# Kernel tuning notes

Hardware: AMD Instinct MI355X
Metric: run time of the kernel (lower is better)

Reference implementation:

```python
import jax, jax.numpy as jnp
import numpy as np

B = 2048          # number of graphs in the batch
ACT_DIM = 14      # nodes per graph (act_dim)
C = 128           # in_channels
H = 256           # hidden_size


def _pair_edges(n):
    ii, jj = np.meshgrid(np.arange(n), np.arange(n), indexing='ij')
    m = ii != jj
    return np.stack([ii[m], jj[m]], axis=1)  # [n*(n-1), 2]


def setup_inputs() -> dict:
    key = jax.random.key(0)
    ks = jax.random.split(key, 12)
    edges_np = _pair_edges(ACT_DIM)                       # [182, 2]
    offs = (np.arange(B) * ACT_DIM)[:, None, None]
    batched = (edges_np[None] + offs).reshape(-1, 2)      # [B*182, 2]
    edge_index = jnp.asarray(batched.T, dtype=jnp.int64 if jax.config.jax_enable_x64 else jnp.int32)
    edges = jnp.asarray(edges_np, dtype=jnp.int32)

    def lin(k, o, i):
        return jax.random.normal(k, (o, i), jnp.float32) * (1.0 / np.sqrt(i))

    return {
        'state': jax.random.normal(ks[0], (B * ACT_DIM, C), jnp.float32),
        'conv_w': lin(ks[1], C, C),
        'conv_b': jnp.zeros((C,), jnp.float32),
        'lin1_w': lin(ks[2], H, 2 * C),
        'lin1_b': jax.random.normal(ks[3], (H,), jnp.float32) * 0.01,
        'lin2_w': lin(ks[4], H, H),
        'lin2_b': jax.random.normal(ks[5], (H,), jnp.float32) * 0.01,
        'mu_w': lin(ks[6], 1, H),
        'mu_b': jnp.zeros((1,), jnp.float32),
        'sig_w': lin(ks[7], 1, H),
        'sig_b': jnp.zeros((1,), jnp.float32),
        'noise': jax.random.normal(ks[8], (B, edges_np.shape[0]), jnp.float32),
        'edge_index': edge_index,
        'edges': edges,
    }


def _gcn_conv(x, edge_index, w, b):
    # Standard GCNConv: add self-loops, symmetric normalization, x @ W^T, scatter-add, + bias.
    n = x.shape[0]
    loops = jnp.arange(n, dtype=edge_index.dtype)
    src = jnp.concatenate([edge_index[0], loops])
    dst = jnp.concatenate([edge_index[1], loops])
    deg = jax.ops.segment_sum(jnp.ones_like(src, dtype=x.dtype), dst, num_segments=n)
    dinv = jax.lax.rsqrt(deg)  # deg >= 1 because of self-loops
    norm = dinv[src] * dinv[dst]                       # [E+N]
    xw = x @ w.T                                       # [N, C]
    msg = xw[src] * norm[:, None]                      # gather + scale
    return jax.ops.segment_sum(msg, dst, num_segments=n) + b


def reference(state, conv_w, conv_b, lin1_w, lin1_b, lin2_w, lin2_b,
              mu_w, mu_b, sig_w, sig_b, noise, edge_index, edges):
    out = jax.nn.relu(_gcn_conv(state, edge_index, conv_w, conv_b))
    x = (out + state).reshape(-1, ACT_DIM, C)          # [B, 14, C]
    es, ed = edges[:, 0], edges[:, 1]
    ef = jnp.concatenate([x[:, es, :], x[:, ed, :]], axis=2)   # [B, E, 2C]
    h = jax.nn.leaky_relu(jnp.einsum('bec,hc->beh', ef, lin1_w) + lin1_b)
    h = jax.nn.leaky_relu(jnp.einsum('beh,gh->beg', h, lin2_w) + lin2_b)
    mu = jax.nn.softplus(jnp.einsum('beh,oh->beo', h, mu_w) + mu_b)[..., 0]   # [B, E]
    std = jax.nn.softplus(jnp.einsum('beh,oh->beo', h, sig_w) + sig_b)[..., 0]
    action = mu + std * noise                          # Normal rsample with fixed eps
    log_prob = jnp.sum(
        -0.5 * ((action - mu) / std) ** 2 - jnp.log(std) - 0.5 * jnp.log(2.0 * jnp.pi),
        axis=-1)                                       # [B]
    return action, log_prob
```

## Files before the change

### kernel.cpp

```cpp
#include <hip/hip_runtime.h>

#define ACT 14
#define CC 128
#define HH 256
#define EPB 182
#define NB 2048
#define M2 (NB*EPB)
#define NS 520
#define LP_CONST (-182.0f * 0.91893853320467274f)

typedef short s16x8 __attribute__((ext_vector_type(8)));
typedef _Float16 h16x8 __attribute__((ext_vector_type(8)));
typedef _Float16 h16x2 __attribute__((ext_vector_type(2)));
typedef float f32x2 __attribute__((ext_vector_type(2)));
typedef float f32x4 __attribute__((ext_vector_type(4)));
typedef int   i32x4 __attribute__((ext_vector_type(4)));
typedef float f32x16 __attribute__((ext_vector_type(16)));

__device__ __forceinline__ float softplusf(float x) { return x > 15.f ? x : log1pf(expf(x)); }

__device__ __forceinline__ short f2h(float f) {
    _Float16 h = (_Float16)f;
    return __builtin_bit_cast(short, h);
}
__device__ __forceinline__ int pk_f16(float a, float b) {
    return __builtin_bit_cast(int, __builtin_amdgcn_cvt_pkrtz(a, b));
}
__device__ __forceinline__ int pk_f16_rn(float a, float b) {
    return (int)(unsigned short)f2h(a) | ((int)f2h(b) << 16);
}
__device__ __forceinline__ float fdot2i(int a, int b, float c) {
#if __has_builtin(__builtin_amdgcn_fdot2)
    return __builtin_amdgcn_fdot2(__builtin_bit_cast(h16x2, a),
                                  __builtin_bit_cast(h16x2, b), c, false);
#else
    h16x2 av = __builtin_bit_cast(h16x2, a), bv = __builtin_bit_cast(h16x2, b);
    return c + (float)av[0] * (float)bv[0] + (float)av[1] * (float)bv[1];
#endif
}

__global__ __launch_bounds__(256) void prep_kernel(
    const float* __restrict__ conv_w, const float* __restrict__ lin1_w,
    const float* __restrict__ lin2_w,
    short* __restrict__ W2h, short* __restrict__ W1h,
    int* __restrict__ cwPT, int* __restrict__ w1sPT)
{
    int i = blockIdx.x * 256 + threadIdx.x;
    W2h[i] = f2h(lin2_w[i]);
    {
        int n = i >> 7, k = i & 127;
        float v = (n < 256) ? lin1_w[n * 256 + k] : lin1_w[(n - 256) * 256 + 128 + k];
        W1h[i] = f2h(v);
    }
    if (i < 8192) {
        int j = i >> 6, p = i & 63;
        cwPT[i] = pk_f16_rn(conv_w[j * 128 + 2 * p], conv_w[j * 128 + 2 * p + 1]);
    }
    if (i < 16384) {
        int h = i >> 6, p = i & 63;
        float a0 = lin1_w[h * 256 + 2 * p]     + lin1_w[h * 256 + 128 + 2 * p];
        float a1 = lin1_w[h * 256 + 2 * p + 1] + lin1_w[h * 256 + 128 + 2 * p + 1];
        w1sPT[i] = pk_f16_rn(a0, a1);
    }
}

__global__ __launch_bounds__(512, 4) void actor_kernel(
    const float* __restrict__ state, const short* __restrict__ W1h,
    const short* __restrict__ W2h,
    const int* __restrict__ cwPT, const float* __restrict__ conv_b,
    const int* __restrict__ w1sPT, const float* __restrict__ lin1_b,
    const float* __restrict__ lin2_b,
    const float* __restrict__ mu_w, const float* __restrict__ sig_w,
    const float* __restrict__ mu_b, const float* __restrict__ sig_b,
    const float* __restrict__ noise, const int* __restrict__ edges,
    float* __restrict__ out)
{
    __shared__ short h1L[2][8192];
    __shared__ short nodeL[2 * ACT * NS];
    __shared__ int   ssP[2][64];
    __shared__ int   gP[2][64];
    __shared__ float wL[2][256];
    __shared__ float b2L[256];
    __shared__ float muL[256], sgL[256];
    __shared__ float mu_acc[384], sg_acc[384];
    __shared__ float lp_acc[2];

    short* stateL = &h1L[0][0];

    const int t = threadIdx.x, b = blockIdx.x;
    const int lane = t & 63, ln = lane & 15, q = lane >> 4;
    const int w = t >> 6;
    const int l32 = lane & 31, hf = lane >> 5;

    #pragma unroll
    for (int it = 0; it < 2; ++it) {
        int idx = it * 512 + t;
        int bt = idx >> 9, row = (idx >> 5) & 15, c4 = idx & 31;
        int kk = c4 >> 3, k8 = (c4 & 7) * 4;
        int* dst = (int*)&stateL[bt * 2560 + kk * 640 + row * 40 + k8];
        if (row < ACT) {
            f32x4 x = *(const f32x4*)(state + ((size_t)(2 * b + bt) * ACT + row) * CC + c4 * 4);
            dst[0] = pk_f16(x[0], x[1]); dst[1] = pk_f16(x[2], x[3]);
        } else { dst[0] = 0; dst[1] = 0; }
    }
    if (t < 256) {
        b2L[t] = lin2_b[t];
        muL[t] = mu_w[t];
        sgL[t] = sig_w[t];
    } else {
        int i = t - 256, bt = i >> 7, c = i & 127;
        const float* sp = state + (size_t)(2 * b + bt) * ACT * CC + c;
        float s = 0.f;
        #pragma unroll
        for (int r = 0; r < ACT; ++r) s += sp[r * CC];
        s *= (1.f / 14.f);
        float s2 = __shfl_xor(s, 1);
        if (!(c & 1)) ssP[bt][c >> 1] = pk_f16(s, s2);
    }
    if (t < 384) { mu_acc[t] = 0.f; sg_acc[t] = 0.f; }
    if (t < 2) lp_acc[t] = 0.f;
    __syncthreads();

    {
        int bt = t >> 8, r = t & 255, j = r >> 1, s = r & 1;
        const i32x4* wp = (const i32x4*)&cwPT[j * 64 + s * 32];
        const i32x4* sp4 = (const i32x4*)&ssP[bt][s * 32];
        float a0 = 0.f, a1 = 0.f, a2 = 0.f, a3 = 0.f;
        #pragma unroll
        for (int u = 0; u < 8; ++u) {
            i32x4 wv = wp[u]; i32x4 sv = sp4[u];
            a0 = fdot2i(wv[0], sv[0], a0); a1 = fdot2i(wv[1], sv[1], a1);
            a2 = fdot2i(wv[2], sv[2], a2); a3 = fdot2i(wv[3], sv[3], a3);
        }
        float a = (a0 + a1) + (a2 + a3);
        a += __shfl_xor(a, 1);
        float gf = fmaxf(a + conv_b[j], 0.f);
        float go = __shfl_xor(gf, 2);
        if ((r & 3) == 0) gP[bt][r >> 2] = pk_f16(gf, go);
    }
    __syncthreads();
    {
        int bt = t >> 8, h = t & 255;
        const i32x4* wp = (const i32x4*)&w1sPT[h * 64];
        const i32x4* gp4 = (const i32x4*)&gP[bt][0];
        float a0 = 0.f, a1 = 0.f, a2 = 0.f, a3 = 0.f;
        #pragma unroll 8
        for (int u = 0; u < 16; ++u) {
            i32x4 wv = wp[u]; i32x4 gv = gp4[u];
            a0 = fdot2i(wv[0], gv[0], a0); a1 = fdot2i(wv[1], gv[1], a1);
            a2 = fdot2i(wv[2], gv[2], a2); a3 = fdot2i(wv[3], gv[3], a3);
        }
        wL[bt][h] = (a0 + a1) + (a2 + a3) + lin1_b[h];
    }
    __syncthreads();

    f32x4 zero4 = {0.f, 0.f, 0.f, 0.f};
    f32x4 nacc[2][4];
    #pragma unroll
    for (int bt = 0; bt < 2; ++bt) {
        nacc[bt][0] = zero4; nacc[bt][1] = zero4;
        nacc[bt][2] = zero4; nacc[bt][3] = zero4;
    }
    #pragma unroll
    for (int c = 0; c < 4; ++c) {
        h16x8 a80 = __builtin_bit_cast(h16x8, *(const s16x8*)&stateL[0 * 2560 + c * 640 + ln * 40 + q * 8]);
        h16x8 a81 = __builtin_bit_cast(h16x8, *(const s16x8*)&stateL[1 * 2560 + c * 640 + ln * 40 + q * 8]);
        #pragma unroll
        for (int i = 0; i < 4; ++i) {
            int ct = w + 8 * i;
            h16x8 b8 = __builtin_bit_cast(h16x8, *(const s16x8*)&W1h[(size_t)(ct * 16 + ln) * CC + c * 32 + q * 8]);
            nacc[0][i] = __builtin_amdgcn_mfma_f32_16x16x32_f16(a80, b8, nacc[0][i], 0, 0, 0);
            nacc[1][i] = __builtin_amdgcn_mfma_f32_16x16x32_f16(a81, b8, nacc[1][i], 0, 0, 0);
        }
    }
    #pragma unroll
    for (int bt = 0; bt < 2; ++bt)
        #pragma unroll
        for (int i = 0; i < 4; ++i) {
            int col = (w + 8 * i) * 16 + ln;
            float wadd = (col < HH) ? wL[bt][col] : 0.f;
            #pragma unroll
            for (int rg = 0; rg < 4; ++rg) {
                int node = q * 4 + rg;
                if (node < ACT) nodeL[(bt * ACT + node) * NS + col] = f2h(nacc[bt][i][rg] + wadd);
            }
        }

    s16x8 wa[16];
    #pragma unroll
    for (int c = 0; c < 16; ++c)
        wa[c] = *(const s16x8*)&W2h[(size_t)(w * 32 + l32) * HH + c * 16 + hf * 8];
    __syncthreads();

    const h16x2 c001 = {(_Float16)0.01f, (_Float16)0.01f};
    auto build = [&](int tile, int bufi) {
        int bt = (tile >= 6) ? 1 : 0;
        int e32 = t & 31;
        int e = (tile - bt * 6) * 32 + e32;
        bool ok = e < EPB;
        int base = bt * ACT * NS;
        int uo = base, vo = base + HH;
        if (ok) { int2 p = ((const int2*)edges)[e]; uo += p.x * NS; vo += p.y * NS; }
        int sl = t >> 5;
        #pragma unroll
        for (int s = 0; s < 2; ++s) {
            int slot = sl + 16 * s;
            int chunk = slot >> 1, half = slot & 1;
            int koff = chunk * 16 + half * 8;
            int o[4] = {0, 0, 0, 0};
            if (ok) {
                s16x8 u8 = *(const s16x8*)&nodeL[uo + koff];
                s16x8 v8 = *(const s16x8*)&nodeL[vo + koff];
                const int* ui = (const int*)&u8;
                const int* vi = (const int*)&v8;
                #pragma unroll
                for (int j = 0; j < 4; ++j) {
                    h16x2 uu = __builtin_bit_cast(h16x2, ui[j]);
                    h16x2 vv = __builtin_bit_cast(h16x2, vi[j]);
                    h16x2 sum = uu + vv;
                    h16x2 lk  = __builtin_elementwise_max(sum, sum * c001);
                    o[j] = __builtin_bit_cast(int, lk);
                }
            }
            *(s16x8*)&h1L[bufi][chunk * 512 + (half * 32 + e32) * 8] = *(const s16x8*)o;
        }
    };

    const f32x2 c001p = {0.01f, 0.01f};
    build(0, 0);
    for (int tile = 0; tile < 12; ++tile) {
        __syncthreads();
        if (tile < 11) build(tile + 1, (tile + 1) & 1);
        const int buf = tile & 1;
        f32x16 acc;
        #pragma unroll
        for (int r = 0; r < 16; ++r) acc[r] = 0.f;
        #pragma unroll
        for (int c = 0; c < 16; ++c) {
            h16x8 b8 = __builtin_bit_cast(h16x8, *(const s16x8*)&h1L[buf][c * 512 + lane * 8]);
            h16x8 a8 = __builtin_bit_cast(h16x8, wa[c]);
            acc = __builtin_amdgcn_mfma_f32_32x32x16_f16(a8, b8, acc, 0, 0, 0);
        }
        int bt = (tile >= 6) ? 1 : 0;
        int col0 = (tile - bt * 6) * 32;
        f32x2 pm = {0.f, 0.f}, ps = {0.f, 0.f};
        const int nsb = w * 32 + 4 * hf;
        #pragma unroll
        for (int g = 0; g < 4; ++g) {
            f32x4 b4 = *(const f32x4*)&b2L[nsb + 8 * g];
            f32x4 m4 = *(const f32x4*)&muL[nsb + 8 * g];
            f32x4 s4 = *(const f32x4*)&sgL[nsb + 8 * g];
            #pragma unroll
            for (int p = 0; p < 2; ++p) {
                f32x2 a2 = {acc[g * 4 + 2 * p], acc[g * 4 + 2 * p + 1]};
                f32x2 b2 = {b4[2 * p], b4[2 * p + 1]};
                f32x2 x  = a2 + b2;
                f32x2 lk = __builtin_elementwise_max(x, x * c001p);
                f32x2 mm = {m4[2 * p], m4[2 * p + 1]};
                f32x2 sv = {s4[2 * p], s4[2 * p + 1]};
                pm += mm * lk;
                ps += sv * lk;
            }
        }
        float pmu = pm[0] + pm[1];
        float psg = ps[0] + ps[1];
        pmu += __shfl_xor(pmu, 32);
        psg += __shfl_xor(psg, 32);
        if (lane < 32) atomicAdd(&mu_acc[bt * 192 + col0 + l32], pmu);
        else           atomicAdd(&sg_acc[bt * 192 + col0 + l32], psg);
    }
    __syncthreads();

    float lpv = 0.f;
    {
        int bt = t >> 8, i = t & 255;
        if (i < EPB) {
            float mu = softplusf(mu_acc[bt * 192 + i] + mu_b[0]);
            float sd = softplusf(sg_acc[bt * 192 + i] + sig_b[0]);
            float z = noise[(size_t)(2 * b + bt) * EPB + i];
            out[(size_t)(2 * b + bt) * EPB + i] = mu + sd * z;
            lpv = -0.5f * z * z - logf(sd);
        }
    }
    #pragma unroll
    for (int off = 1; off < 64; off <<= 1) lpv += __shfl_xor(lpv, off);
    if (lane == 0) atomicAdd(&lp_acc[t >> 8], lpv);
    __syncthreads();
    if (t < 2) out[M2 + 2 * b + t] = lp_acc[t] + LP_CONST;
}

extern "C" void kernel_launch(void* const* d_in, const int* in_sizes, int n_in,
                              void* d_out, int out_size, void* d_ws, size_t ws_size,
                              hipStream_t stream)
{
    const float* state  = (const float*)d_in[0];
    const float* conv_w = (const float*)d_in[1];
    const float* conv_b = (const float*)d_in[2];
    const float* lin1_w = (const float*)d_in[3];
    const float* lin1_b = (const float*)d_in[4];
    const float* lin2_w = (const float*)d_in[5];
    const float* lin2_b = (const float*)d_in[6];
    const float* mu_w   = (const float*)d_in[7];
    const float* mu_b   = (const float*)d_in[8];
    const float* sig_w  = (const float*)d_in[9];
    const float* sig_b  = (const float*)d_in[10];
    const float* noise  = (const float*)d_in[11];
    const int*   edges  = (const int*)d_in[13];
    float* out = (float*)d_out;

    char* ws = (char*)d_ws;
    short* W2h    = (short*)ws;  ws += 65536 * 2;
    short* W1h    = (short*)ws;  ws += 65536 * 2;
    int*   cwPT   = (int*)ws;    ws += 8192 * 4;
    int*   w1sPT  = (int*)ws;    ws += 16384 * 4;

    prep_kernel<<<256, 256, 0, stream>>>(conv_w, lin1_w, lin2_w,
                                         W2h, W1h, cwPT, w1sPT);
    actor_kernel<<<NB / 2, 512, 0, stream>>>(state, W1h, W2h,
                                             cwPT, conv_b, w1sPT, lin1_b,
                                             lin2_b, mu_w, sig_w, mu_b, sig_b,
                                             noise, edges, out);
}
```

Baseline: 205.1 us.

## Build edge-feature MFMA operands in registers instead of staging through LDS

```diff
diff --git a/kernel.cpp b/kernel.cpp
--- a/kernel.cpp
+++ b/kernel.cpp
@@ -75,7 +75,7 @@
     const float* __restrict__ noise, const int* __restrict__ edges,
     float* __restrict__ out)
 {
-    __shared__ short h1L[2][8192];
+    __shared__ short stateL[2 * 2560];
     __shared__ short nodeL[2 * ACT * NS];
     __shared__ int   ssP[2][64];
     __shared__ int   gP[2][64];
@@ -84,8 +84,6 @@
     __shared__ float muL[256], sgL[256];
     __shared__ float mu_acc[384], sg_acc[384];
     __shared__ float lp_acc[2];
-
-    short* stateL = &h1L[0][0];
 
     const int t = threadIdx.x, b = blockIdx.x;
     const int lane = t & 63, ln = lane & 15, q = lane >> 4;
@@ -193,56 +191,39 @@
     __syncthreads();
 
     const h16x2 c001 = {(_Float16)0.01f, (_Float16)0.01f};
-    auto build = [&](int tile, int bufi) {
-        int bt = (tile >= 6) ? 1 : 0;
-        int e32 = t & 31;
-        int e = (tile - bt * 6) * 32 + e32;
-        bool ok = e < EPB;
-        int base = bt * ACT * NS;
-        int uo = base, vo = base + HH;
-        if (ok) { int2 p = ((const int2*)edges)[e]; uo += p.x * NS; vo += p.y * NS; }
-        int sl = t >> 5;
-        #pragma unroll
-        for (int s = 0; s < 2; ++s) {
-            int slot = sl + 16 * s;
-            int chunk = slot >> 1, half = slot & 1;
-            int koff = chunk * 16 + half * 8;
-            int o[4] = {0, 0, 0, 0};
-            if (ok) {
-                s16x8 u8 = *(const s16x8*)&nodeL[uo + koff];
-                s16x8 v8 = *(const s16x8*)&nodeL[vo + koff];
-                const int* ui = (const int*)&u8;
-                const int* vi = (const int*)&v8;
-                #pragma unroll
-                for (int j = 0; j < 4; ++j) {
-                    h16x2 uu = __builtin_bit_cast(h16x2, ui[j]);
-                    h16x2 vv = __builtin_bit_cast(h16x2, vi[j]);
-                    h16x2 sum = uu + vv;
-                    h16x2 lk  = __builtin_elementwise_max(sum, sum * c001);
-                    o[j] = __builtin_bit_cast(int, lk);
-                }
+    const f32x2 c001p = {0.01f, 0.01f};
+    for (int tile = 0; tile < 12; ++tile) {
+        const int bt = (tile >= 6) ? 1 : 0;
+        const int col0 = (tile - bt * 6) * 32;
+        int e = col0 + l32;
+        if (e > EPB - 1) e = EPB - 1;
+        int2 p = ((const int2*)edges)[e];
+        const int base = bt * ACT * NS;
+        const int uo = base + p.x * NS + hf * 8;
+        const int vo = base + HH + p.y * NS + hf * 8;
+
+        f32x16 acc;
+        #pragma unroll
+        for (int r = 0; r < 16; ++r) acc[r] = 0.f;
+        #pragma unroll
+        for (int c = 0; c < 16; ++c) {
+            s16x8 u8 = *(const s16x8*)&nodeL[uo + c * 16];
+            s16x8 v8 = *(const s16x8*)&nodeL[vo + c * 16];
+            const int* ui = (const int*)&u8;
+            const int* vi = (const int*)&v8;
+            i32x4 o;
+            #pragma unroll
+            for (int j = 0; j < 4; ++j) {
+                h16x2 uu = __builtin_bit_cast(h16x2, ui[j]);
+                h16x2 vv = __builtin_bit_cast(h16x2, vi[j]);
+                h16x2 sum = uu + vv;
+                h16x2 lk  = __builtin_elementwise_max(sum, sum * c001);
+                o[j] = __builtin_bit_cast(int, lk);
             }
-            *(s16x8*)&h1L[bufi][chunk * 512 + (half * 32 + e32) * 8] = *(const s16x8*)o;
-        }
-    };
-
-    const f32x2 c001p = {0.01f, 0.01f};
-    build(0, 0);
-    for (int tile = 0; tile < 12; ++tile) {
-        __syncthreads();
-        if (tile < 11) build(tile + 1, (tile + 1) & 1);
-        const int buf = tile & 1;
-        f32x16 acc;
-        #pragma unroll
-        for (int r = 0; r < 16; ++r) acc[r] = 0.f;
-        #pragma unroll
-        for (int c = 0; c < 16; ++c) {
-            h16x8 b8 = __builtin_bit_cast(h16x8, *(const s16x8*)&h1L[buf][c * 512 + lane * 8]);
+            h16x8 b8 = __builtin_bit_cast(h16x8, o);
             h16x8 a8 = __builtin_bit_cast(h16x8, wa[c]);
             acc = __builtin_amdgcn_mfma_f32_32x32x16_f16(a8, b8, acc, 0, 0, 0);
         }
-        int bt = (tile >= 6) ? 1 : 0;
-        int col0 = (tile - bt * 6) * 32;
         f32x2 pm = {0.f, 0.f}, ps = {0.f, 0.f};
         const int nsb = w * 32 + 4 * hf;
         #pragma unroll
@@ -251,13 +232,13 @@
             f32x4 m4 = *(const f32x4*)&muL[nsb + 8 * g];
             f32x4 s4 = *(const f32x4*)&sgL[nsb + 8 * g];
             #pragma unroll
-            for (int p = 0; p < 2; ++p) {
-                f32x2 a2 = {acc[g * 4 + 2 * p], acc[g * 4 + 2 * p + 1]};
-                f32x2 b2 = {b4[2 * p], b4[2 * p + 1]};
+            for (int pp = 0; pp < 2; ++pp) {
+                f32x2 a2 = {acc[g * 4 + 2 * pp], acc[g * 4 + 2 * pp + 1]};
+                f32x2 b2 = {b4[2 * pp], b4[2 * pp + 1]};
                 f32x2 x  = a2 + b2;
                 f32x2 lk = __builtin_elementwise_max(x, x * c001p);
-                f32x2 mm = {m4[2 * p], m4[2 * p + 1]};
-                f32x2 sv = {s4[2 * p], s4[2 * p + 1]};
+                f32x2 mm = {m4[2 * pp], m4[2 * pp + 1]};
+                f32x2 sv = {s4[2 * pp], s4[2 * pp + 1]};
                 pm += mm * lk;
                 ps += sv * lk;
             }
```

New measurement: 235.5 us. 14.8% more time.
